# Kernel tuning notes

Hardware: AMD Instinct MI355X
Metric: run time of the kernel (lower is better)

## Reference

```python
import jax, jax.numpy as jnp
import numpy as np

B = 256      # batch
ZD = 128     # z_dim
HIN = 128    # H_inputs
H = 512      # hidden
HT = 32      # H_t
N = 16384    # num nodes
RW = 16      # rw_len
TEMP = 1.0
P_DROP = 0.2
EPS_C = 0.1  # constraints epsilon


def setup_inputs() -> dict:
    key = jax.random.key(0)
    ks = jax.random.split(key, 20)
    def w(k, shape, fan):
        return (jax.random.normal(k, shape, jnp.float32) / np.float32(np.sqrt(fan)))
    z = lambda n: jnp.zeros((n,), jnp.float32)
    u = jax.random.uniform(ks[14], (RW, B, N), jnp.float32)
    return {
        "latent": jax.random.normal(ks[0], (B, ZD + 1), jnp.float32),
        "inputs0": jnp.zeros((B, HIN), jnp.float32),
        "Wc": w(ks[1], (ZD, ZD + 1), ZD + 1), "bc": z(ZD),
        "Ws": w(ks[2], (H, ZD), ZD), "bs": z(H),
        "Wh": w(ks[3], (H, H), H), "bh": z(H),
        "Wcc": w(ks[4], (H, H), H), "bcc": z(H),
        "W_ih": w(ks[5], (4 * H, HIN), HIN), "b_ih": z(4 * H),
        "W_hh": w(ks[6], (4 * H, H), H), "b_hh": z(4 * H),
        "W_up": w(ks[7], (N, H), H), "b_up": z(N),
        "W_down": w(ks[8], (HIN, N), N),
        "Wt_down": w(ks[9], (HT, H), H), "bt_down": z(HT),
        "Wt_pred": w(ks[10], (1, HT), HT),
        "Wt_up": w(ks[11], (HT, 1), 1), "bt_up": z(HT),
        "W_vt": w(ks[12], (HIN, HIN + HT), HIN + HT),
        "W_prob": w(ks[13], (1, HIN), HIN),
        # pre-sampled Gumbel noise per step (torch.rand -> gumbel)
        "gumbel": -jnp.log(-jnp.log(u + 1e-20) + 1e-20),
        # uniforms for dropout masks in TimeDecoder (forced train mode)
        "drop_u": jax.random.uniform(ks[15], (RW, B, HT), jnp.float32),
    }


def reference(latent, inputs0, Wc, bc, Ws, bs, Wh, bh, Wcc, bcc,
              W_ih, b_ih, W_hh, b_hh, W_up, b_up, W_down,
              Wt_down, bt_down, Wt_pred, Wt_up, bt_up, W_vt, W_prob,
              gumbel, drop_u):
    # induced=True path: compress latent, init (h, c)
    lat = jnp.tanh(latent @ Wc.T + bc)               # [B, ZD]
    s = jnp.tanh(lat @ Ws.T + bs)                    # [B, H]
    h0 = jnp.tanh(s @ Wh.T + bh)
    c0 = jnp.tanh(s @ Wcc.T + bcc)
    keep = 1.0 - P_DROP

    def step(carry, xs):
        x, h, c, last_t = carry
        g, du = xs
        # torch LSTMCell: gate order i, f, g, o
        gates = x @ W_ih.T + b_ih + h @ W_hh.T + b_hh  # [B, 4H]
        i, f, gg, o = jnp.split(gates, 4, axis=1)
        c2 = jax.nn.sigmoid(f) * c + jax.nn.sigmoid(i) * jnp.tanh(gg)
        h2 = jax.nn.sigmoid(o) * jnp.tanh(c2)
        # node logits + gumbel-softmax sample
        p = h2 @ W_up.T + b_up                         # [B, N]
        v = jax.nn.softmax((p + g) / TEMP, axis=1)
        Hg = v @ W_down.T                              # [B, HIN]
        # TimeDecoder (dropout always in train mode)
        td = jnp.tanh(h2 @ Wt_down.T + bt_down)        # [B, HT]
        td = td * (du < keep).astype(td.dtype) / keep
        t = jnp.minimum(td @ Wt_pred.T, 1.0)           # [B, 1]
        # constraints(t, last_t)
        mn = jnp.min(t)
        t = jnp.where(mn < EPS_C, t - mn, t)
        mx = jnp.max(t)
        t = jnp.where(mx > 1.0, t / mx, t)
        t = jnp.clip(t, last_t, 1.0)
        Ht = t @ Wt_up.T + bt_up                       # [B, HT]
        x2 = jnp.concatenate([Hg, Ht], axis=1) @ W_vt.T  # [B, HIN]
        return (x2, h2, c2, t), (v, t)

    last_t0 = jnp.zeros((latent.shape[0], 1), latent.dtype)
    (xf, _, _, _), (rw, ts) = jax.lax.scan(step, (inputs0, h0, c0, last_t0), (gumbel, drop_u))
    rw = jnp.transpose(rw, (1, 0, 2))   # [B, RW, N]
    ts = jnp.transpose(ts, (1, 0, 2))   # [B, RW, 1]
    prob = xf @ W_prob.T                # [B, 1]
    return rw, ts, prob
```

## Files before the change

kernel.cpp:

```cpp
#include <hip/hip_runtime.h>

typedef float  __attribute__((ext_vector_type(4))) f32x4;
typedef int    __attribute__((ext_vector_type(4))) i32x4;
typedef unsigned short u16;

#define B    256
#define H    512
#define HIN  128
#define N    16384
#define RW   16
#define HT   32
#define KC2  672
#define HOFF 160
#define RWN  262144
#define TS_OFF   67108864
#define PROB_OFF 67112960

__device__ __forceinline__ u16 f2bf(float f) {
  unsigned u = __builtin_bit_cast(unsigned, f);
  u += 0x7FFFu + ((u >> 16) & 1u);
  return (u16)(u >> 16);
}
__device__ __forceinline__ float bf2f(u16 v) {
  return __builtin_bit_cast(float, ((unsigned)v) << 16);
}
__device__ __forceinline__ float sigm(float x) { return 1.0f / (1.0f + expf(-x)); }

__device__ __forceinline__ void mfma(f32x4& d, i32x4 a, i32x4 b) {
  asm volatile("v_mfma_f32_16x16x32_bf16 %0, %1, %2, %0" : "+v"(d) : "v"(a), "v"(b));
}
__device__ __forceinline__ void mfma_n(f32x4& d, i32x4 a, i32x4 b) {
  asm volatile("s_nop 1\n\tv_mfma_f32_16x16x32_bf16 %0, %1, %2, %0" : "+v"(d) : "v"(a), "v"(b));
}
__device__ __forceinline__ void fence_acc(f32x4& v) {
  asm volatile("s_nop 7\n\ts_nop 7" : "+v"(v));
}

__global__ __launch_bounds__(256) void k_prep(
    const float* __restrict__ W_up, const float* __restrict__ W_down,
    const float* __restrict__ W_hh, const float* __restrict__ Wt_down,
    const float* __restrict__ b_ih, const float* __restrict__ b_hh,
    const float* __restrict__ Wh, const float* __restrict__ Wcc,
    u16* __restrict__ Wup_b, u16* __restrict__ Wdn_b, u16* __restrict__ Wfull,
    u16* __restrict__ Wtd_b, u16* __restrict__ Whc_b,
    float* __restrict__ bcomb, u16* __restrict__ xcat0, float* __restrict__ tstep)
{
  const int idx0 = blockIdx.x * 256 + threadIdx.x;
  const int stride = gridDim.x * 256;
  for (int i = idx0; i < N * H; i += stride) Wup_b[i] = f2bf(W_up[i]);
  for (int i = idx0; i < HIN * N; i += stride) Wdn_b[i] = f2bf(W_down[i]);
  for (int i = idx0; i < 4 * H * H; i += stride) {
    int j = i >> 9, k = i & 511;
    Wfull[j * KC2 + HOFF + k] = f2bf(W_hh[i]);
  }
  for (int i = idx0; i < HT * H; i += stride) Wtd_b[i] = f2bf(Wt_down[i]);
  for (int i = idx0; i < 2 * H * H; i += stride) {
    int j = i >> 9, k = i & 511;
    Whc_b[i] = f2bf(j < H ? Wh[j * H + k] : Wcc[(j - H) * H + k]);
  }
  for (int i = idx0; i < 4 * H; i += stride) bcomb[i] = b_ih[i] + b_hh[i];
  for (int i = idx0; i < B * HOFF; i += stride) {
    int b = i / HOFF, m = i - b * HOFF;
    xcat0[b * KC2 + m] = 0;
  }
  for (int i = idx0; i < B; i += stride) tstep[i] = 0.0f;
}

__global__ __launch_bounds__(256) void k_fold(
    const float* __restrict__ W_ih, const float* __restrict__ W_vt,
    const float* __restrict__ inputs0, const float* __restrict__ W_prob,
    u16* __restrict__ Wfull, float* __restrict__ g0add, float* __restrict__ wpc)
{
  int idx = blockIdx.x * 256 + threadIdx.x;
  if (idx < 2048 * 160) {
    int j = idx / 160, m = idx - j * 160;
    float a = 0.0f;
    for (int c = 0; c < HIN; ++c) a += W_ih[j * HIN + c] * W_vt[c * 160 + m];
    Wfull[j * KC2 + m] = f2bf(a);
  } else if (idx < 2048 * 160 + 256 * 2048) {
    int i2 = idx - 2048 * 160;
    int b = i2 >> 11, j = i2 & 2047;
    float a = 0.0f;
    for (int k = 0; k < HIN; ++k) a += inputs0[b * HIN + k] * W_ih[j * HIN + k];
    g0add[i2] = a;
  } else if (idx < 2048 * 160 + 256 * 2048 + 160) {
    int m = idx - (2048 * 160 + 256 * 2048);
    float a = 0.0f;
    for (int k = 0; k < HIN; ++k) a += W_prob[k] * W_vt[k * 160 + m];
    wpc[m] = a;
  }
}

__global__ __launch_bounds__(256) void k_lat(
    const float* __restrict__ latent, const float* __restrict__ Wc,
    const float* __restrict__ bc, float* __restrict__ latbuf)
{
  int idx = blockIdx.x * 256 + threadIdx.x;
  int b = idx >> 7, i = idx & 127;
  float acc = bc[i];
  for (int k = 0; k < 129; ++k) acc += latent[b * 129 + k] * Wc[i * 129 + k];
  latbuf[idx] = tanhf(acc);
}

__global__ __launch_bounds__(256) void k_sinit(
    const float* __restrict__ latbuf, const float* __restrict__ Ws,
    const float* __restrict__ bs, u16* __restrict__ sinit_b)
{
  int idx = blockIdx.x * 256 + threadIdx.x;
  int b = idx >> 9, j = idx & 511;
  float acc = bs[j];
  for (int k = 0; k < HIN; ++k) acc += latbuf[b * HIN + k] * Ws[j * HIN + k];
  sinit_b[idx] = f2bf(tanhf(acc));
}

__global__ __launch_bounds__(256) void k_h0c0m(
    const u16* __restrict__ sinit_b, const u16* __restrict__ Whc_b,
    const float* __restrict__ bh, const float* __restrict__ bcc,
    float* __restrict__ cbuf, u16* __restrict__ xc0)
{
  const int rb = blockIdx.x >> 6, cb = blockIdx.x & 63;
  const int wave = threadIdx.x >> 6, lane = threadIdx.x & 63;
  const int lr = lane & 15, lk = lane >> 4;
  const int m0 = rb * 16, col0 = cb * 16;
  const u16* ab = sinit_b + (m0 + lr) * H + wave * 128 + 8 * lk;
  const u16* bb = Whc_b + (col0 + lr) * H + wave * 128 + 8 * lk;
  f32x4 acc[2] = {};
  mfma_n(acc[0], *(const i32x4*)(ab),      *(const i32x4*)(bb));
  mfma_n(acc[1], *(const i32x4*)(ab + 32), *(const i32x4*)(bb + 32));
  mfma(acc[0], *(const i32x4*)(ab + 64), *(const i32x4*)(bb + 64));
  mfma(acc[1], *(const i32x4*)(ab + 96), *(const i32x4*)(bb + 96));
  fence_acc(acc[0]); fence_acc(acc[1]);
  __shared__ float q[4][16][17];
  #pragma unroll
  for (int rr = 0; rr < 4; ++rr)
    q[wave][4 * lk + rr][lr] = acc[0][rr] + acc[1][rr];
  __syncthreads();
  const int r2 = threadIdx.x >> 4, jj = threadIdx.x & 15;
  float s = q[0][r2][jj] + q[1][r2][jj] + q[2][r2][jj] + q[3][r2][jj];
  int col = col0 + jj;
  if (col < H) xc0[(m0 + r2) * KC2 + HOFF + col] = f2bf(tanhf(s + bh[col]));
  else         cbuf[(m0 + r2) * H + col - H]     = tanhf(s + bcc[col - H]);
}

__global__ __launch_bounds__(256) void k_lstm(
    const u16* __restrict__ xc, const u16* __restrict__ Wfull,
    const float* __restrict__ bcomb, float* __restrict__ cbuf,
    u16* __restrict__ xn, const float* __restrict__ g0, float* __restrict__ rowL)
{
  if (blockIdx.x == 0) rowL[threadIdx.x] = 0.0f;
  const int rb = blockIdx.x >> 5, cb = blockIdx.x & 31;
  const int wave = threadIdx.x >> 6, lane = threadIdx.x & 63;
  const int lr = lane & 15, lk = lane >> 4;
  const int m0 = rb * 16, j0 = cb * 16;
  const int gcol = wave * H + j0 + lr;
  f32x4 acc[2] = {};
  const u16* brow = Wfull + gcol * KC2 + 8 * lk;
  const u16* arow = xc + (m0 + lr) * KC2 + 8 * lk;
  mfma_n(acc[0], *(const i32x4*)(arow),      *(const i32x4*)(brow));
  mfma_n(acc[1], *(const i32x4*)(arow + 32), *(const i32x4*)(brow + 32));
  #pragma unroll 4
  for (int i = 2; i < 21; ++i) {
    int kk = i * 32;
    mfma(acc[i & 1], *(const i32x4*)(arow + kk), *(const i32x4*)(brow + kk));
  }
  fence_acc(acc[0]); fence_acc(acc[1]);
  __shared__ float q[4][16][17];
  float bias = bcomb[gcol];
  #pragma unroll
  for (int rr = 0; rr < 4; ++rr)
    q[wave][4 * lk + rr][lr] = acc[0][rr] + acc[1][rr] + bias;
  __syncthreads();
  const int r2 = threadIdx.x >> 4, jj = threadIdx.x & 15;
  const int b = m0 + r2, j = j0 + jj;
  float gi = q[0][r2][jj], gf = q[1][r2][jj], gg = q[2][r2][jj], go = q[3][r2][jj];
  if (g0) {
    const float* gp = g0 + b * 2048 + j;
    gi += gp[0]; gf += gp[512]; gg += gp[1024]; go += gp[1536];
  }
  float c  = cbuf[b * H + j];
  float c2 = sigm(gf) * c + sigm(gi) * tanhf(gg);
  float h2 = sigm(go) * tanhf(c2);
  cbuf[b * H + j] = c2;
  xn[b * KC2 + HOFF + j] = f2bf(h2);
}

__global__ __launch_bounds__(256) void k_pgemm(
    const u16* __restrict__ xin, const u16* __restrict__ Wup,
    const float* __restrict__ b_up, const float* __restrict__ gum,
    float* __restrict__ out_rw, float* __restrict__ rowL,
    u16* __restrict__ HgPart, const u16* __restrict__ Wdn,
    const u16* __restrict__ Wtd, const float* __restrict__ bt_down,
    const float* __restrict__ Wt_pred, const float* __restrict__ du,
    float* __restrict__ t0, int r)
{
  const int rb = blockIdx.x >> 7, cb = blockIdx.x & 127;
  const int wave = threadIdx.x >> 6, lane = threadIdx.x & 63;
  const int lr = lane & 15, lk = lane >> 4;
  const int m0 = rb * 32;
  const int n0 = cb * 128 + wave * 32;

  float gv[2][4][2], bup0 = b_up[n0 + lr], bup1 = b_up[n0 + 16 + lr];
  #pragma unroll
  for (int mi = 0; mi < 2; ++mi)
    #pragma unroll
    for (int rr = 0; rr < 4; ++rr) {
      int row = m0 + 16 * mi + 4 * lk + rr;
      gv[mi][rr][0] = gum[(size_t)row * N + n0 + lr];
      gv[mi][rr][1] = gum[(size_t)row * N + n0 + 16 + lr];
    }

  f32x4 acc[2][2] = {};
  const u16* a0 = xin + (m0 + lr) * KC2 + HOFF + 8 * lk;
  const u16* a1 = a0 + 16 * KC2;
  const u16* b0 = Wup + (n0 + lr) * H + 8 * lk;
  const u16* b1 = b0 + 16 * H;
  {
    i32x4 af0 = *(const i32x4*)(a0);
    i32x4 af1 = *(const i32x4*)(a1);
    i32x4 bf0 = *(const i32x4*)(b0);
    i32x4 bf1 = *(const i32x4*)(b1);
    mfma_n(acc[0][0], af0, bf0); mfma_n(acc[0][1], af0, bf1);
    mfma_n(acc[1][0], af1, bf0); mfma_n(acc[1][1], af1, bf1);
  }
  #pragma unroll 3
  for (int kk = 32; kk < H; kk += 32) {
    i32x4 af0 = *(const i32x4*)(a0 + kk);
    i32x4 af1 = *(const i32x4*)(a1 + kk);
    i32x4 bf0 = *(const i32x4*)(b0 + kk);
    i32x4 bf1 = *(const i32x4*)(b1 + kk);
    mfma(acc[0][0], af0, bf0); mfma(acc[0][1], af0, bf1);
    mfma(acc[1][0], af1, bf0); mfma(acc[1][1], af1, bf1);
  }
  #pragma unroll
  for (int mi = 0; mi < 2; ++mi) { fence_acc(acc[mi][0]); fence_acc(acc[mi][1]); }

  __shared__ float eL[32][132];
  __shared__ float sL[4][32];
  #pragma unroll
  for (int mi = 0; mi < 2; ++mi)
    #pragma unroll
    for (int rr = 0; rr < 4; ++rr) {
      int rl = 16 * mi + 4 * lk + rr;
      int row = m0 + rl;
      float* sp = out_rw + (size_t)row * RWN + (size_t)r * N + n0 + lr;
      float v0 = acc[mi][0][rr] + bup0 + gv[mi][rr][0];
      float v1 = acc[mi][1][rr] + bup1 + gv[mi][rr][1];
      float e0 = expf(fminf(v0, 80.0f));
      float e1 = expf(fminf(v1, 80.0f));
      sp[0] = e0; sp[16] = e1;
      eL[rl][wave * 32 + lr] = e0;
      eL[rl][wave * 32 + 16 + lr] = e1;
      float par = e0 + e1;
      #pragma unroll
      for (int off = 1; off < 16; off <<= 1) par += __shfl_xor(par, off);
      if (lr == 0) sL[wave][rl] = par;
    }
  __syncthreads();
  if (threadIdx.x < 32)
    atomicAdd(rowL + m0 + threadIdx.x,
              sL[0][threadIdx.x] + sL[1][threadIdx.x] + sL[2][threadIdx.x] + sL[3][threadIdx.x]);

  const int nb = cb * 128;
  f32x4 acc2[2][2] = {};
  #pragma unroll
  for (int kk2 = 0; kk2 < 4; ++kk2) {
    i32x4 af[2];
    #pragma unroll
    for (int mi2 = 0; mi2 < 2; ++mi2) {
      const float* ep = &eL[16 * mi2 + lr][kk2 * 32 + 8 * lk];
      f32x4 x0 = *(const f32x4*)ep;
      f32x4 x1 = *(const f32x4*)(ep + 4);
      af[mi2][0] = (int)f2bf(x0[0]) | ((int)f2bf(x0[1]) << 16);
      af[mi2][1] = (int)f2bf(x0[2]) | ((int)f2bf(x0[3]) << 16);
      af[mi2][2] = (int)f2bf(x1[0]) | ((int)f2bf(x1[1]) << 16);
      af[mi2][3] = (int)f2bf(x1[2]) | ((int)f2bf(x1[3]) << 16);
    }
    i32x4 bf0 = *(const i32x4*)(Wdn + (size_t)(wave * 32 + lr) * N + nb + kk2 * 32 + 8 * lk);
    i32x4 bf1 = *(const i32x4*)(Wdn + (size_t)(wave * 32 + 16 + lr) * N + nb + kk2 * 32 + 8 * lk);
    mfma_n(acc2[0][0], af[0], bf0); mfma_n(acc2[0][1], af[0], bf1);
    mfma_n(acc2[1][0], af[1], bf0); mfma_n(acc2[1][1], af[1], bf1);
  }
  #pragma unroll
  for (int mi2 = 0; mi2 < 2; ++mi2) { fence_acc(acc2[mi2][0]); fence_acc(acc2[mi2][1]); }
  u16* hp = HgPart + (size_t)cb * (B * HIN);
  #pragma unroll
  for (int mi2 = 0; mi2 < 2; ++mi2)
    #pragma unroll
    for (int ni = 0; ni < 2; ++ni)
      #pragma unroll
      for (int rr = 0; rr < 4; ++rr)
        hp[(m0 + 16 * mi2 + 4 * lk + rr) * HIN + wave * 32 + 16 * ni + lr] =
            f2bf(acc2[mi2][ni][rr]);

  if (cb == 0 && wave < 2) {
    f32x4 acc3[2] = {};
    const u16* at = xin + (m0 + wave * 16 + lr) * KC2 + HOFF + 8 * lk;
    {
      i32x4 af = *(const i32x4*)(at);
      mfma_n(acc3[0], af, *(const i32x4*)(Wtd + lr * H + 8 * lk));
      mfma_n(acc3[1], af, *(const i32x4*)(Wtd + (16 + lr) * H + 8 * lk));
    }
    for (int kk = 32; kk < H; kk += 32) {
      i32x4 af = *(const i32x4*)(at + kk);
      mfma(acc3[0], af, *(const i32x4*)(Wtd + lr * H + kk + 8 * lk));
      mfma(acc3[1], af, *(const i32x4*)(Wtd + (16 + lr) * H + kk + 8 * lk));
    }
    fence_acc(acc3[0]); fence_acc(acc3[1]);
    float wp0 = Wt_pred[lr],  wp1 = Wt_pred[16 + lr];
    float bt0 = bt_down[lr],  bt1 = bt_down[16 + lr];
    #pragma unroll
    for (int rr = 0; rr < 4; ++rr) {
      int row = m0 + wave * 16 + 4 * lk + rr;
      float td0 = tanhf(acc3[0][rr] + bt0);
      float td1 = tanhf(acc3[1][rr] + bt1);
      td0 = (du[row * HT + lr]      < 0.8f) ? td0 * 1.25f : 0.0f;
      td1 = (du[row * HT + 16 + lr] < 0.8f) ? td1 * 1.25f : 0.0f;
      float part = td0 * wp0 + td1 * wp1;
      #pragma unroll
      for (int off = 1; off < 16; off <<= 1) part += __shfl_xor(part, off);
      if (lr == 0) t0[row] = fminf(part, 1.0f);
    }
  }
}

__global__ __launch_bounds__(256) void k_vscale(
    float* __restrict__ out_rw, const float* __restrict__ rowL,
    const u16* __restrict__ HgPart, const float* __restrict__ t0,
    float* __restrict__ tstep, const float* __restrict__ Wt_up,
    const float* __restrict__ bt_up, float* __restrict__ ts_out,
    u16* __restrict__ xn, float* __restrict__ Hgf, int r)
{
  const int b = blockIdx.x, tid = threadIdx.x;
  const int rg = b >> 7, cb = b & 127;
  const int row = rg * 16 + (tid >> 4);
  const int coff = (tid & 15) * 8;
  const float R = 1.0f / rowL[row];
  float* orow = out_rw + (size_t)row * RWN + (size_t)r * N + cb * 128 + coff;
  f32x4 x0 = *(const f32x4*)orow;
  f32x4 x1 = *(const f32x4*)(orow + 4);
  #pragma unroll
  for (int e = 0; e < 4; ++e) { x0[e] *= R; x1[e] *= R; }
  *(f32x4*)orow = x0;
  *(f32x4*)(orow + 4) = x1;

  if ((b & 15) == 8) {
    const int idx = (b >> 4) * 256 + tid;
    float s0 = 0.f, s1 = 0.f, s2 = 0.f, s3 = 0.f;
    #pragma unroll 4
    for (int c = 0; c < 128; c += 4) {
      s0 += bf2f(HgPart[(size_t)(c + 0) * (B * HIN) + idx]);
      s1 += bf2f(HgPart[(size_t)(c + 1) * (B * HIN) + idx]);
      s2 += bf2f(HgPart[(size_t)(c + 2) * (B * HIN) + idx]);
      s3 += bf2f(HgPart[(size_t)(c + 3) * (B * HIN) + idx]);
    }
    float hg = ((s0 + s1) + (s2 + s3)) / rowL[idx >> 7];
    Hgf[idx] = hg;
    xn[(idx >> 7) * KC2 + (idx & 127)] = f2bf(hg);
  }

  if (b == 2047) {
    __shared__ float red[256];
    float tv = t0[tid];
    red[tid] = tv; __syncthreads();
    for (int s = 128; s > 0; s >>= 1) {
      if (tid < s) red[tid] = fminf(red[tid], red[tid + s]);
      __syncthreads();
    }
    float mn = red[0]; __syncthreads();
    if (mn < 0.1f) tv -= mn;
    red[tid] = tv; __syncthreads();
    for (int s = 128; s > 0; s >>= 1) {
      if (tid < s) red[tid] = fmaxf(red[tid], red[tid + s]);
      __syncthreads();
    }
    float mx = red[0];
    if (mx > 1.0f) tv /= mx;
    tv = fminf(fmaxf(tv, tstep[r * B + tid]), 1.0f);
    tstep[(r + 1) * B + tid] = tv;
    ts_out[tid * RW + r] = tv;
    #pragma unroll 4
    for (int j = 0; j < HT; ++j)
      xn[tid * KC2 + HIN + j] = f2bf(tv * Wt_up[j] + bt_up[j]);
  }
}

__global__ __launch_bounds__(256) void k_prob(
    const float* __restrict__ Hgf, const float* __restrict__ tstep,
    const float* __restrict__ Wt_up, const float* __restrict__ bt_up,
    const float* __restrict__ wpc, float* __restrict__ outp)
{
  int b = threadIdx.x;
  float acc = 0.0f;
  for (int m = 0; m < HIN; ++m) acc += Hgf[b * HIN + m] * wpc[m];
  float tv = tstep[16 * B + b];
  for (int j = 0; j < HT; ++j) acc += (tv * Wt_up[j] + bt_up[j]) * wpc[HIN + j];
  outp[b] = acc;
}

extern "C" void kernel_launch(void* const* d_in, const int* in_sizes, int n_in,
                              void* d_out, int out_size, void* d_ws, size_t ws_size,
                              hipStream_t stream) {
  (void)in_sizes; (void)n_in; (void)out_size; (void)ws_size;
  const float* latent  = (const float*)d_in[0];
  const float* inputs0 = (const float*)d_in[1];
  const float* Wc      = (const float*)d_in[2];
  const float* bc      = (const float*)d_in[3];
  const float* Ws      = (const float*)d_in[4];
  const float* bs      = (const float*)d_in[5];
  const float* Wh      = (const float*)d_in[6];
  const float* bh      = (const float*)d_in[7];
  const float* Wcc     = (const float*)d_in[8];
  const float* bcc     = (const float*)d_in[9];
  const float* W_ih    = (const float*)d_in[10];
  const float* b_ih    = (const float*)d_in[11];
  const float* W_hh    = (const float*)d_in[12];
  const float* b_hh    = (const float*)d_in[13];
  const float* W_up    = (const float*)d_in[14];
  const float* b_up    = (const float*)d_in[15];
  const float* W_down  = (const float*)d_in[16];
  const float* Wt_down = (const float*)d_in[17];
  const float* bt_down = (const float*)d_in[18];
  const float* Wt_pred = (const float*)d_in[19];
  const float* Wt_up   = (const float*)d_in[20];
  const float* bt_up   = (const float*)d_in[21];
  const float* W_vt    = (const float*)d_in[22];
  const float* W_prob  = (const float*)d_in[23];
  const float* gumbel  = (const float*)d_in[24];
  const float* drop_u  = (const float*)d_in[25];
  float* out = (float*)d_out;

  char* p = (char*)d_ws;
  auto alloc = [&](size_t bytes) { char* r = p; p += (bytes + 255) & ~(size_t)255; return r; };
  u16*   Wup_b  = (u16*)  alloc((size_t)N * H * 2);
  u16*   Wdn_b  = (u16*)  alloc((size_t)HIN * N * 2);
  u16*   Wfull_b= (u16*)  alloc((size_t)4 * H * KC2 * 2);
  u16*   Wtd_b  = (u16*)  alloc((size_t)HT * H * 2);
  u16*   Whc_b  = (u16*)  alloc((size_t)2 * H * H * 2);
  float* bcomb  = (float*)alloc(4 * H * 4);
  u16*   xcat0  = (u16*)  alloc((size_t)B * KC2 * 2);
  u16*   xcat1  = (u16*)  alloc((size_t)B * KC2 * 2);
  float* cbuf   = (float*)alloc((size_t)B * H * 4);
  u16*   sinit_b= (u16*)  alloc((size_t)B * H * 2);
  float* latbuf = (float*)alloc((size_t)B * HIN * 4);
  float* rowL   = (float*)alloc(B * 4);
  float* t0buf  = (float*)alloc(B * 4);
  float* tstep  = (float*)alloc((size_t)17 * B * 4);
  u16*   HgPart = (u16*)  alloc((size_t)128 * B * HIN * 2);
  float* Hgf    = (float*)alloc((size_t)B * HIN * 4);
  float* g0add  = (float*)alloc((size_t)B * 4 * H * 4);
  float* wpc    = (float*)alloc(160 * 4);

  k_prep<<<2048, 256, 0, stream>>>(W_up, W_down, W_hh, Wt_down, b_ih, b_hh, Wh, Wcc,
                                   Wup_b, Wdn_b, Wfull_b, Wtd_b, Whc_b, bcomb, xcat0, tstep);
  k_fold<<<3330, 256, 0, stream>>>(W_ih, W_vt, inputs0, W_prob, Wfull_b, g0add, wpc);
  k_lat  <<<128, 256, 0, stream>>>(latent, Wc, bc, latbuf);
  k_sinit<<<512, 256, 0, stream>>>(latbuf, Ws, bs, sinit_b);
  k_h0c0m<<<1024, 256, 0, stream>>>(sinit_b, Whc_b, bh, bcc, cbuf, xcat0);

  for (int r = 0; r < 16; ++r) {
    u16* xc = (r & 1) ? xcat1 : xcat0;
    u16* xn = (r & 1) ? xcat0 : xcat1;
    k_lstm <<<512, 256, 0, stream>>>(xc, Wfull_b, bcomb, cbuf, xn,
                                     r == 0 ? g0add : (const float*)nullptr, rowL);
    k_pgemm<<<1024, 256, 0, stream>>>(xn, Wup_b, b_up, gumbel + (size_t)r * B * N,
                                      out, rowL, HgPart, Wdn_b,
                                      Wtd_b, bt_down, Wt_pred, drop_u + (size_t)r * B * HT,
                                      t0buf, r);
    k_vscale<<<2048, 256, 0, stream>>>(out, rowL, HgPart, t0buf, tstep, Wt_up, bt_up,
                                       out + TS_OFF, xn, Hgf, r);
  }
  k_prob<<<1, 256, 0, stream>>>(Hgf, tstep, Wt_up, bt_up, wpc, out + PROB_OFF);
}
```

Before: 1.294 ms.

## Fuse per-step kernels into one cooperative persistent kernel with grid barriers

Replaces the 48 per-step launches (lstm, pgemm, vscale) with a single cooperative kernel of 1024 blocks that loops over all 16 steps, separated by a hierarchical atomic grid barrier. Softmax exponentials are staged in bf16 double buffers and normalized into the output one step later, overlapped with the next step's logits GEMM. The per-row sum buffers become per-step arrays to allow this. Launch overhead and per-kernel tail gaps are meant to go away, in exchange for barrier spin costs, the occupancy of 1024 co-resident blocks, and an extra bf16 round trip for the probabilities.

Measured after the change: 4.872 ms. +276.7%, slower.

```diff
diff --git a/kernel.cpp b/kernel.cpp
--- a/kernel.cpp
+++ b/kernel.cpp
@@ -15,6 +15,9 @@
 #define RWN  262144
 #define TS_OFF   67108864
 #define PROB_OFF 67112960
+#define NBLK 1024
+#define NGRP 32
+#define GRPSZ (NBLK / NGRP)
 
 __device__ __forceinline__ u16 f2bf(float f) {
   unsigned u = __builtin_bit_cast(unsigned, f);
@@ -34,6 +37,41 @@
 }
 __device__ __forceinline__ void fence_acc(f32x4& v) {
   asm volatile("s_nop 7\n\ts_nop 7" : "+v"(v));
+}
+
+__device__ __forceinline__ void gsync(unsigned* bar) {
+  __syncthreads();
+  if (threadIdx.x == 0) {
+    __threadfence();
+    const int g = blockIdx.x & (NGRP - 1);
+    unsigned t = __hip_atomic_fetch_add(bar + g * 32, 1u, __ATOMIC_ACQ_REL, __HIP_MEMORY_SCOPE_AGENT);
+    if (((t + 1) & (GRPSZ - 1)) == 0)
+      __hip_atomic_fetch_add(bar + NGRP * 32, 1u, __ATOMIC_ACQ_REL, __HIP_MEMORY_SCOPE_AGENT);
+    unsigned target = (t / GRPSZ + 1) * NGRP;
+    while (__hip_atomic_load(bar + NGRP * 32, __ATOMIC_RELAXED, __HIP_MEMORY_SCOPE_AGENT) < target)
+      __builtin_amdgcn_s_sleep(2);
+    __threadfence();
+  }
+  __syncthreads();
+}
+
+__device__ __forceinline__ void norm_slice(const u16* __restrict__ ebp,
+                                           const float* __restrict__ rowLp,
+                                           float* __restrict__ out, int slot,
+                                           int blk, int tid) {
+  #pragma unroll
+  for (int uu = 0; uu < 4; ++uu) {
+    int flat = (blk * 1024 + uu * 256 + tid) * 4;
+    int row = flat >> 14;
+    float Rv = 1.0f / rowLp[row];
+    unsigned long long ev = *(const unsigned long long*)(ebp + flat);
+    f32x4 o;
+    o[0] = bf2f((u16)ev) * Rv;
+    o[1] = bf2f((u16)(ev >> 16)) * Rv;
+    o[2] = bf2f((u16)(ev >> 32)) * Rv;
+    o[3] = bf2f((u16)(ev >> 48)) * Rv;
+    *(f32x4*)(out + (size_t)row * RWN + (size_t)slot * N + (flat & (N - 1))) = o;
+  }
 }
 
 __global__ __launch_bounds__(256) void k_prep(
@@ -43,7 +81,8 @@
     const float* __restrict__ Wh, const float* __restrict__ Wcc,
     u16* __restrict__ Wup_b, u16* __restrict__ Wdn_b, u16* __restrict__ Wfull,
     u16* __restrict__ Wtd_b, u16* __restrict__ Whc_b,
-    float* __restrict__ bcomb, u16* __restrict__ xcat0, float* __restrict__ tstep)
+    float* __restrict__ bcomb, u16* __restrict__ xcat0, float* __restrict__ tstep,
+    unsigned* __restrict__ bar)
 {
   const int idx0 = blockIdx.x * 256 + threadIdx.x;
   const int stride = gridDim.x * 256;
@@ -64,6 +103,7 @@
     xcat0[b * KC2 + m] = 0;
   }
   for (int i = idx0; i < B; i += stride) tstep[i] = 0.0f;
+  for (int i = idx0; i < 2048; i += stride) bar[i] = 0;
 }
 
 __global__ __launch_bounds__(256) void k_fold(
@@ -142,7 +182,270 @@
   else         cbuf[(m0 + r2) * H + col - H]     = tanhf(s + bcc[col - H]);
 }
 
-__global__ __launch_bounds__(256) void k_lstm(
+__global__ __launch_bounds__(256, 4) void k_mega(
+    const u16* __restrict__ Wfull, const float* __restrict__ bcomb,
+    float* __restrict__ cbuf, u16* __restrict__ xcat0, u16* __restrict__ xcat1,
+    const u16* __restrict__ Wup, const float* __restrict__ b_up,
+    const float* __restrict__ gumbel, const u16* __restrict__ Wdn,
+    u16* __restrict__ ebuf0, u16* __restrict__ ebuf1,
+    float* __restrict__ rowLs, u16* __restrict__ HgPart,
+    const u16* __restrict__ Wtd, const float* __restrict__ bt_down,
+    const float* __restrict__ Wt_pred, const float* __restrict__ du_all,
+    float* __restrict__ t0buf, float* __restrict__ tstep,
+    const float* __restrict__ Wt_up, const float* __restrict__ bt_up,
+    const float* __restrict__ g0add, const float* __restrict__ wpc,
+    float* __restrict__ Hgf, float* __restrict__ out, unsigned* __restrict__ bar)
+{
+  __shared__ float smf[32 * 132 + 4 * 32];
+  const int blk = blockIdx.x, tid = threadIdx.x;
+  const int wave = tid >> 6, lane = tid & 63;
+  const int lr = lane & 15, lk = lane >> 4;
+
+  for (int r = 0; r < 16; ++r) {
+    const u16* xc = (r & 1) ? xcat1 : xcat0;
+    u16* xn = (r & 1) ? xcat0 : xcat1;
+    float* rowL = rowLs + r * B;
+    u16* eb = (r & 1) ? ebuf1 : ebuf0;
+    const u16* ebp = (r & 1) ? ebuf0 : ebuf1;
+
+    if (blk < 512) {
+      if (blk == 0) rowL[tid] = 0.0f;
+      const int rb = blk >> 5, cb = blk & 31;
+      const int m0 = rb * 16, j0 = cb * 16;
+      const int gcol = wave * H + j0 + lr;
+      f32x4 acc[2] = {};
+      const u16* brow = Wfull + gcol * KC2 + 8 * lk;
+      const u16* arow = xc + (m0 + lr) * KC2 + 8 * lk;
+      mfma_n(acc[0], *(const i32x4*)(arow),      *(const i32x4*)(brow));
+      mfma_n(acc[1], *(const i32x4*)(arow + 32), *(const i32x4*)(brow + 32));
+      #pragma unroll 4
+      for (int i = 2; i < 21; ++i) {
+        int kk = i * 32;
+        mfma(acc[i & 1], *(const i32x4*)(arow + kk), *(const i32x4*)(brow + kk));
+      }
+      fence_acc(acc[0]); fence_acc(acc[1]);
+      float bias = bcomb[gcol];
+      #pragma unroll
+      for (int rr = 0; rr < 4; ++rr)
+        smf[(wave * 16 + 4 * lk + rr) * 17 + lr] = acc[0][rr] + acc[1][rr] + bias;
+      __syncthreads();
+      const int r2 = tid >> 4, jj = tid & 15;
+      const int bb = m0 + r2, j = j0 + jj;
+      float gi = smf[(r2) * 17 + jj],       gf = smf[(16 + r2) * 17 + jj];
+      float gg = smf[(32 + r2) * 17 + jj],  go = smf[(48 + r2) * 17 + jj];
+      if (r == 0) {
+        const float* gp = g0add + bb * 2048 + j;
+        gi += gp[0]; gf += gp[512]; gg += gp[1024]; go += gp[1536];
+      }
+      float c  = cbuf[bb * H + j];
+      float c2 = sigm(gf) * c + sigm(gi) * tanhf(gg);
+      float h2 = sigm(go) * tanhf(c2);
+      cbuf[bb * H + j] = c2;
+      xn[bb * KC2 + HOFF + j] = f2bf(h2);
+    }
+    gsync(bar);
+
+    {
+      const int rb = blk >> 7, cb = blk & 127;
+      const int m0 = rb * 32;
+      const int n0 = cb * 128 + wave * 32;
+      const float* gum = gumbel + (size_t)r * B * N;
+
+      float gv[2][4][2], bup0 = b_up[n0 + lr], bup1 = b_up[n0 + 16 + lr];
+      #pragma unroll
+      for (int mi = 0; mi < 2; ++mi)
+        #pragma unroll
+        for (int rr = 0; rr < 4; ++rr) {
+          int row = m0 + 16 * mi + 4 * lk + rr;
+          gv[mi][rr][0] = gum[(size_t)row * N + n0 + lr];
+          gv[mi][rr][1] = gum[(size_t)row * N + n0 + 16 + lr];
+        }
+
+      f32x4 acc[2][2] = {};
+      const u16* a0 = xn + (m0 + lr) * KC2 + HOFF + 8 * lk;
+      const u16* a1 = a0 + 16 * KC2;
+      const u16* b0 = Wup + (n0 + lr) * H + 8 * lk;
+      const u16* b1 = b0 + 16 * H;
+      {
+        i32x4 af0 = *(const i32x4*)(a0);
+        i32x4 af1 = *(const i32x4*)(a1);
+        i32x4 bf0 = *(const i32x4*)(b0);
+        i32x4 bf1 = *(const i32x4*)(b1);
+        mfma_n(acc[0][0], af0, bf0); mfma_n(acc[0][1], af0, bf1);
+        mfma_n(acc[1][0], af1, bf0); mfma_n(acc[1][1], af1, bf1);
+      }
+      #pragma unroll 3
+      for (int kk = 32; kk < H; kk += 32) {
+        i32x4 af0 = *(const i32x4*)(a0 + kk);
+        i32x4 af1 = *(const i32x4*)(a1 + kk);
+        i32x4 bf0 = *(const i32x4*)(b0 + kk);
+        i32x4 bf1 = *(const i32x4*)(b1 + kk);
+        mfma(acc[0][0], af0, bf0); mfma(acc[0][1], af0, bf1);
+        mfma(acc[1][0], af1, bf0); mfma(acc[1][1], af1, bf1);
+      }
+      #pragma unroll
+      for (int mi = 0; mi < 2; ++mi) { fence_acc(acc[mi][0]); fence_acc(acc[mi][1]); }
+
+      float* eLf = smf;
+      float* sLf = smf + 32 * 132;
+      #pragma unroll
+      for (int mi = 0; mi < 2; ++mi)
+        #pragma unroll
+        for (int rr = 0; rr < 4; ++rr) {
+          int rl = 16 * mi + 4 * lk + rr;
+          int row = m0 + rl;
+          u16* sp = eb + (size_t)row * N + n0 + lr;
+          float v0 = acc[mi][0][rr] + bup0 + gv[mi][rr][0];
+          float v1 = acc[mi][1][rr] + bup1 + gv[mi][rr][1];
+          float e0 = expf(fminf(v0, 80.0f));
+          float e1 = expf(fminf(v1, 80.0f));
+          sp[0] = f2bf(e0); sp[16] = f2bf(e1);
+          eLf[rl * 132 + wave * 32 + lr] = e0;
+          eLf[rl * 132 + wave * 32 + 16 + lr] = e1;
+          float par = e0 + e1;
+          #pragma unroll
+          for (int off = 1; off < 16; off <<= 1) par += __shfl_xor(par, off);
+          if (lr == 0) sLf[wave * 32 + rl] = par;
+        }
+      __syncthreads();
+      if (tid < 32)
+        atomicAdd(rowL + m0 + tid, sLf[tid] + sLf[32 + tid] + sLf[64 + tid] + sLf[96 + tid]);
+
+      const int nb = cb * 128;
+      f32x4 acc2[2][2] = {};
+      #pragma unroll
+      for (int kk2 = 0; kk2 < 4; ++kk2) {
+        i32x4 af[2];
+        #pragma unroll
+        for (int mi2 = 0; mi2 < 2; ++mi2) {
+          const float* ep = &eLf[(16 * mi2 + lr) * 132 + kk2 * 32 + 8 * lk];
+          f32x4 x0 = *(const f32x4*)ep;
+          f32x4 x1 = *(const f32x4*)(ep + 4);
+          af[mi2][0] = (int)f2bf(x0[0]) | ((int)f2bf(x0[1]) << 16);
+          af[mi2][1] = (int)f2bf(x0[2]) | ((int)f2bf(x0[3]) << 16);
+          af[mi2][2] = (int)f2bf(x1[0]) | ((int)f2bf(x1[1]) << 16);
+          af[mi2][3] = (int)f2bf(x1[2]) | ((int)f2bf(x1[3]) << 16);
+        }
+        i32x4 bf0 = *(const i32x4*)(Wdn + (size_t)(wave * 32 + lr) * N + nb + kk2 * 32 + 8 * lk);
+        i32x4 bf1 = *(const i32x4*)(Wdn + (size_t)(wave * 32 + 16 + lr) * N + nb + kk2 * 32 + 8 * lk);
+        mfma_n(acc2[0][0], af[0], bf0); mfma_n(acc2[0][1], af[0], bf1);
+        mfma_n(acc2[1][0], af[1], bf0); mfma_n(acc2[1][1], af[1], bf1);
+      }
+      #pragma unroll
+      for (int mi2 = 0; mi2 < 2; ++mi2) { fence_acc(acc2[mi2][0]); fence_acc(acc2[mi2][1]); }
+      u16* hp = HgPart + (size_t)cb * (B * HIN);
+      #pragma unroll
+      for (int mi2 = 0; mi2 < 2; ++mi2)
+        #pragma unroll
+        for (int ni = 0; ni < 2; ++ni)
+          #pragma unroll
+          for (int rr = 0; rr < 4; ++rr)
+            hp[(m0 + 16 * mi2 + 4 * lk + rr) * HIN + wave * 32 + 16 * ni + lr] =
+                f2bf(acc2[mi2][ni][rr]);
+
+      if (cb == 0 && wave < 2) {
+        const float* du = du_all + (size_t)r * B * HT;
+        f32x4 acc3[2] = {};
+        const u16* at = xn + (m0 + wave * 16 + lr) * KC2 + HOFF + 8 * lk;
+        {
+          i32x4 af = *(const i32x4*)(at);
+          mfma_n(acc3[0], af, *(const i32x4*)(Wtd + lr * H + 8 * lk));
+          mfma_n(acc3[1], af, *(const i32x4*)(Wtd + (16 + lr) * H + 8 * lk));
+        }
+        for (int kk = 32; kk < H; kk += 32) {
+          i32x4 af = *(const i32x4*)(at + kk);
+          mfma(acc3[0], af, *(const i32x4*)(Wtd + lr * H + kk + 8 * lk));
+          mfma(acc3[1], af, *(const i32x4*)(Wtd + (16 + lr) * H + kk + 8 * lk));
+        }
+        fence_acc(acc3[0]); fence_acc(acc3[1]);
+        float wp0 = Wt_pred[lr],  wp1 = Wt_pred[16 + lr];
+        float bt0 = bt_down[lr],  bt1 = bt_down[16 + lr];
+        #pragma unroll
+        for (int rr = 0; rr < 4; ++rr) {
+          int row = m0 + wave * 16 + 4 * lk + rr;
+          float td0 = tanhf(acc3[0][rr] + bt0);
+          float td1 = tanhf(acc3[1][rr] + bt1);
+          td0 = (du[row * HT + lr]      < 0.8f) ? td0 * 1.25f : 0.0f;
+          td1 = (du[row * HT + 16 + lr] < 0.8f) ? td1 * 1.25f : 0.0f;
+          float part = td0 * wp0 + td1 * wp1;
+          #pragma unroll
+          for (int off = 1; off < 16; off <<= 1) part += __shfl_xor(part, off);
+          if (lr == 0) t0buf[row] = fminf(part, 1.0f);
+        }
+      }
+
+      if (r > 0) norm_slice(ebp, rowLs + (r - 1) * B, out, r - 1, blk, tid);
+    }
+    gsync(bar);
+
+    {
+      const int i5 = tid & 31, part = tid >> 5;
+      const int idx = blk * 32 + i5;
+      const u16* hp = HgPart + (size_t)part * 16 * (B * HIN) + idx;
+      float a0 = 0.f, a1 = 0.f, a2 = 0.f, a3 = 0.f;
+      #pragma unroll
+      for (int c = 0; c < 16; c += 4) {
+        a0 += bf2f(hp[(size_t)(c + 0) * (B * HIN)]);
+        a1 += bf2f(hp[(size_t)(c + 1) * (B * HIN)]);
+        a2 += bf2f(hp[(size_t)(c + 2) * (B * HIN)]);
+        a3 += bf2f(hp[(size_t)(c + 3) * (B * HIN)]);
+      }
+      smf[part * 32 + i5] = (a0 + a1) + (a2 + a3);
+      __syncthreads();
+      if (tid < 32) {
+        float t = smf[tid];
+        #pragma unroll
+        for (int p2 = 1; p2 < 8; ++p2) t += smf[p2 * 32 + tid];
+        int id2 = blk * 32 + tid;
+        float hg = t / rowL[id2 >> 7];
+        Hgf[id2] = hg;
+        xn[(id2 >> 7) * KC2 + (id2 & 127)] = f2bf(hg);
+      }
+      if (blk == NBLK - 1) {
+        __syncthreads();
+        float* red = smf + 256;
+        float* tl  = smf + 512;
+        float tv = t0buf[tid];
+        red[tid] = tv; __syncthreads();
+        for (int s2 = 128; s2 > 0; s2 >>= 1) {
+          if (tid < s2) red[tid] = fminf(red[tid], red[tid + s2]);
+          __syncthreads();
+        }
+        float mn = red[0]; __syncthreads();
+        if (mn < 0.1f) tv -= mn;
+        red[tid] = tv; __syncthreads();
+        for (int s2 = 128; s2 > 0; s2 >>= 1) {
+          if (tid < s2) red[tid] = fmaxf(red[tid], red[tid + s2]);
+          __syncthreads();
+        }
+        float mx = red[0];
+        if (mx > 1.0f) tv /= mx;
+        tv = fminf(fmaxf(tv, tstep[r * B + tid]), 1.0f);
+        tstep[(r + 1) * B + tid] = tv;
+        out[TS_OFF + tid * RW + r] = tv;
+        tl[tid] = tv; __syncthreads();
+        const int jj = tid & 31, r8 = tid >> 5;
+        #pragma unroll 4
+        for (int g2 = 0; g2 < 32; ++g2) {
+          int row = g2 * 8 + r8;
+          xn[row * KC2 + HIN + jj] = f2bf(tl[row] * Wt_up[jj] + bt_up[jj]);
+        }
+      }
+    }
+    gsync(bar);
+  }
+
+  norm_slice(ebuf1, rowLs + 15 * B, out, 15, blk, tid);
+  if (blk == 0) {
+    float acc = 0.0f;
+    for (int m = 0; m < HIN; ++m) acc += Hgf[tid * HIN + m] * wpc[m];
+    float tv = tstep[16 * B + tid];
+    for (int j = 0; j < HT; ++j) acc += (tv * Wt_up[j] + bt_up[j]) * wpc[HIN + j];
+    out[PROB_OFF + tid] = acc;
+  }
+}
+
+__global__ __launch_bounds__(256) void fb_lstm(
     const u16* __restrict__ xc, const u16* __restrict__ Wfull,
     const float* __restrict__ bcomb, float* __restrict__ cbuf,
     u16* __restrict__ xn, const float* __restrict__ g0, float* __restrict__ rowL)
@@ -184,7 +487,7 @@
   xn[b * KC2 + HOFF + j] = f2bf(h2);
 }
 
-__global__ __launch_bounds__(256) void k_pgemm(
+__global__ __launch_bounds__(256) void fb_pgemm(
     const u16* __restrict__ xin, const u16* __restrict__ Wup,
     const float* __restrict__ b_up, const float* __restrict__ gum,
     float* __restrict__ out_rw, float* __restrict__ rowL,
@@ -198,7 +501,6 @@
   const int lr = lane & 15, lk = lane >> 4;
   const int m0 = rb * 32;
   const int n0 = cb * 128 + wave * 32;
-
   float gv[2][4][2], bup0 = b_up[n0 + lr], bup1 = b_up[n0 + 16 + lr];
   #pragma unroll
   for (int mi = 0; mi < 2; ++mi)
@@ -208,7 +510,6 @@
       gv[mi][rr][0] = gum[(size_t)row * N + n0 + lr];
       gv[mi][rr][1] = gum[(size_t)row * N + n0 + 16 + lr];
     }
-
   f32x4 acc[2][2] = {};
   const u16* a0 = xin + (m0 + lr) * KC2 + HOFF + 8 * lk;
   const u16* a1 = a0 + 16 * KC2;
@@ -233,7 +534,6 @@
   }
   #pragma unroll
   for (int mi = 0; mi < 2; ++mi) { fence_acc(acc[mi][0]); fence_acc(acc[mi][1]); }
-
   __shared__ float eL[32][132];
   __shared__ float sL[4][32];
   #pragma unroll
@@ -259,7 +559,6 @@
   if (threadIdx.x < 32)
     atomicAdd(rowL + m0 + threadIdx.x,
               sL[0][threadIdx.x] + sL[1][threadIdx.x] + sL[2][threadIdx.x] + sL[3][threadIdx.x]);
-
   const int nb = cb * 128;
   f32x4 acc2[2][2] = {};
   #pragma unroll
@@ -291,7 +590,6 @@
       for (int rr = 0; rr < 4; ++rr)
         hp[(m0 + 16 * mi2 + 4 * lk + rr) * HIN + wave * 32 + 16 * ni + lr] =
             f2bf(acc2[mi2][ni][rr]);
-
   if (cb == 0 && wave < 2) {
     f32x4 acc3[2] = {};
     const u16* at = xin + (m0 + wave * 16 + lr) * KC2 + HOFF + 8 * lk;
@@ -323,7 +621,7 @@
   }
 }
 
-__global__ __launch_bounds__(256) void k_vscale(
+__global__ __launch_bounds__(256) void fb_vscale(
     float* __restrict__ out_rw, const float* __restrict__ rowL,
     const u16* __restrict__ HgPart, const float* __restrict__ t0,
     float* __restrict__ tstep, const float* __restrict__ Wt_up,
@@ -342,7 +640,6 @@
   for (int e = 0; e < 4; ++e) { x0[e] *= R; x1[e] *= R; }
   *(f32x4*)orow = x0;
   *(f32x4*)(orow + 4) = x1;
-
   if ((b & 15) == 8) {
     const int idx = (b >> 4) * 256 + tid;
     float s0 = 0.f, s1 = 0.f, s2 = 0.f, s3 = 0.f;
@@ -357,9 +654,8 @@
     Hgf[idx] = hg;
     xn[(idx >> 7) * KC2 + (idx & 127)] = f2bf(hg);
   }
-
   if (b == 2047) {
-    __shared__ float red[256];
+    __shared__ float red[256], tl[256];
     float tv = t0[tid];
     red[tid] = tv; __syncthreads();
     for (int s = 128; s > 0; s >>= 1) {
@@ -378,13 +674,17 @@
     tv = fminf(fmaxf(tv, tstep[r * B + tid]), 1.0f);
     tstep[(r + 1) * B + tid] = tv;
     ts_out[tid * RW + r] = tv;
+    tl[tid] = tv; __syncthreads();
+    const int jj = tid & 31, r8 = tid >> 5;
     #pragma unroll 4
-    for (int j = 0; j < HT; ++j)
-      xn[tid * KC2 + HIN + j] = f2bf(tv * Wt_up[j] + bt_up[j]);
-  }
-}
-
-__global__ __launch_bounds__(256) void k_prob(
+    for (int g2 = 0; g2 < 32; ++g2) {
+      int rw2 = g2 * 8 + r8;
+      xn[rw2 * KC2 + HIN + jj] = f2bf(tl[rw2] * Wt_up[jj] + bt_up[jj]);
+    }
+  }
+}
+
+__global__ __launch_bounds__(256) void fb_prob(
     const float* __restrict__ Hgf, const float* __restrict__ tstep,
     const float* __restrict__ Wt_up, const float* __restrict__ bt_up,
     const float* __restrict__ wpc, float* __restrict__ outp)
@@ -442,32 +742,50 @@
   float* cbuf   = (float*)alloc((size_t)B * H * 4);
   u16*   sinit_b= (u16*)  alloc((size_t)B * H * 2);
   float* latbuf = (float*)alloc((size_t)B * HIN * 4);
-  float* rowL   = (float*)alloc(B * 4);
+  float* rowLs  = (float*)alloc((size_t)16 * B * 4);
   float* t0buf  = (float*)alloc(B * 4);
   float* tstep  = (float*)alloc((size_t)17 * B * 4);
   u16*   HgPart = (u16*)  alloc((size_t)128 * B * HIN * 2);
   float* Hgf    = (float*)alloc((size_t)B * HIN * 4);
   float* g0add  = (float*)alloc((size_t)B * 4 * H * 4);
   float* wpc    = (float*)alloc(160 * 4);
+  u16*   ebuf0  = (u16*)  alloc((size_t)B * N * 2);
+  u16*   ebuf1  = (u16*)  alloc((size_t)B * N * 2);
+  unsigned* bar = (unsigned*)alloc(2048 * 4);
 
   k_prep<<<2048, 256, 0, stream>>>(W_up, W_down, W_hh, Wt_down, b_ih, b_hh, Wh, Wcc,
-                                   Wup_b, Wdn_b, Wfull_b, Wtd_b, Whc_b, bcomb, xcat0, tstep);
+                                   Wup_b, Wdn_b, Wfull_b, Wtd_b, Whc_b, bcomb, xcat0,
+                                   tstep, bar);
   k_fold<<<3330, 256, 0, stream>>>(W_ih, W_vt, inputs0, W_prob, Wfull_b, g0add, wpc);
   k_lat  <<<128, 256, 0, stream>>>(latent, Wc, bc, latbuf);
   k_sinit<<<512, 256, 0, stream>>>(latbuf, Ws, bs, sinit_b);
   k_h0c0m<<<1024, 256, 0, stream>>>(sinit_b, Whc_b, bh, bcc, cbuf, xcat0);
 
-  for (int r = 0; r < 16; ++r) {
-    u16* xc = (r & 1) ? xcat1 : xcat0;
-    u16* xn = (r & 1) ? xcat0 : xcat1;
-    k_lstm <<<512, 256, 0, stream>>>(xc, Wfull_b, bcomb, cbuf, xn,
-                                     r == 0 ? g0add : (const float*)nullptr, rowL);
-    k_pgemm<<<1024, 256, 0, stream>>>(xn, Wup_b, b_up, gumbel + (size_t)r * B * N,
-                                      out, rowL, HgPart, Wdn_b,
-                                      Wtd_b, bt_down, Wt_pred, drop_u + (size_t)r * B * HT,
-                                      t0buf, r);
-    k_vscale<<<2048, 256, 0, stream>>>(out, rowL, HgPart, t0buf, tstep, Wt_up, bt_up,
-                                       out + TS_OFF, xn, Hgf, r);
-  }
-  k_prob<<<1, 256, 0, stream>>>(Hgf, tstep, Wt_up, bt_up, wpc, out + PROB_OFF);
-}
+  void* kargs[] = {
+    (void*)&Wfull_b, (void*)&bcomb, (void*)&cbuf, (void*)&xcat0, (void*)&xcat1,
+    (void*)&Wup_b, (void*)&b_up, (void*)&gumbel, (void*)&Wdn_b,
+    (void*)&ebuf0, (void*)&ebuf1, (void*)&rowLs, (void*)&HgPart,
+    (void*)&Wtd_b, (void*)&bt_down, (void*)&Wt_pred, (void*)&drop_u,
+    (void*)&t0buf, (void*)&tstep, (void*)&Wt_up, (void*)&bt_up,
+    (void*)&g0add, (void*)&wpc, (void*)&Hgf, (void*)&out, (void*)&bar
+  };
+  hipError_t ce = hipLaunchCooperativeKernel(
+      reinterpret_cast<const void*>(&k_mega), dim3(NBLK), dim3(256), kargs, 0, stream);
+
+  if (ce != hipSuccess) {
+    (void)hipGetLastError();
+    for (int r = 0; r < 16; ++r) {
+      u16* xc = (r & 1) ? xcat1 : xcat0;
+      u16* xn = (r & 1) ? xcat0 : xcat1;
+      fb_lstm <<<512, 256, 0, stream>>>(xc, Wfull_b, bcomb, cbuf, xn,
+                                        r == 0 ? g0add : (const float*)nullptr, rowLs);
+      fb_pgemm<<<1024, 256, 0, stream>>>(xn, Wup_b, b_up, gumbel + (size_t)r * B * N,
+                                         out, rowLs, HgPart, Wdn_b,
+                                         Wtd_b, bt_down, Wt_pred,
+                                         drop_u + (size_t)r * B * HT, t0buf, r);
+      fb_vscale<<<2048, 256, 0, stream>>>(out, rowLs, HgPart, t0buf, tstep, Wt_up, bt_up,
+                                          out + TS_OFF, xn, Hgf, r);
+    }
+    fb_prob<<<1, 256, 0, stream>>>(Hgf, tstep, Wt_up, bt_up, wpc, out + PROB_OFF);
+  }
+}
```
